# Kernel tuning notes

Measured on AMD Instinct MI355X. Metric: run time of the kernel, lower is better.

Reference implementation:

```python
import jax, jax.numpy as jnp
import numpy as np

M, N, H, K1, K2, C, B = 100000, 14000, 256, 16, 32, 7, 64
EPS = 1e-8


def setup_inputs() -> dict:
    key = jax.random.key(0)
    ks = jax.random.split(key, 8)
    embeds = jax.random.normal(ks[0], (M, H), dtype=jnp.float32)
    idx = jax.random.randint(ks[1], (N,), 0, M, dtype=jnp.int32)
    neighbors = jax.random.randint(ks[2], (N, K1), 0, M, dtype=jnp.int32)
    neighbors_2hop = jax.random.randint(ks[3], (N, K2), 0, M, dtype=jnp.int32)
    labels = (jnp.arange(N, dtype=jnp.int32) % C)  # perfectly balanced, as averageemb requires
    # prompt params (downstreamprompt weights, xavier-uniform [1,H])
    lim = float(np.sqrt(6.0 / (1 + H)))
    w_self = jax.random.uniform(ks[4], (1, H), jnp.float32, -lim, lim)
    w_n = jax.random.uniform(ks[5], (1, H), jnp.float32, -lim, lim)
    w_n2 = jax.random.uniform(ks[6], (1, H), jnp.float32, -lim, lim)
    # metanet (PromptVector): bottleneck adapter H -> B -> H
    k7, k8 = jax.random.split(ks[7])
    W1 = jax.random.normal(k7, (H, B), jnp.float32) * (1.0 / np.sqrt(H))
    b1 = jnp.zeros((B,), jnp.float32)
    W2 = jax.random.normal(k8, (B, H), jnp.float32) * (1.0 / np.sqrt(B))
    b2 = jnp.zeros((H,), jnp.float32)
    return {"embeds": embeds, "w_self": w_self, "w_n": w_n, "w_n2": w_n2,
            "W1": W1, "b1": b1, "W2": W2, "b2": b2,
            "idx": idx, "neighbors": neighbors, "neighbors_2hop": neighbors_2hop,
            "labels": labels}


def _cos(a, b):
    # torch.cosine_similarity with eps=1e-8 (clamped norms)
    num = jnp.sum(a * b, axis=-1)
    na = jnp.maximum(jnp.sqrt(jnp.sum(a * a, axis=-1)), EPS)
    nb = jnp.maximum(jnp.sqrt(jnp.sum(b * b, axis=-1)), EPS)
    return num / (na * nb)


def reference(embeds, w_self, w_n, w_n2, W1, b1, W2, b2,
              idx, neighbors, neighbors_2hop, labels):
    center = embeds[idx]                         # [N,H]
    ce = w_self * center                         # selfprompt: [N,H]
    nb = jnp.nan_to_num(w_n * embeds[neighbors])              # [N,K1,H]
    nb2 = jnp.nan_to_num(w_n2 * embeds[neighbors_2hop])       # [N,K2,H]
    nb_all = jnp.concatenate([nb, nb2], axis=1)  # [N,K1+K2,H]
    sim = _cos(ce[:, None, :], nb_all)           # [N,K]
    w = jax.nn.softmax(sim, axis=-1)
    weighted_neighbors = jnp.einsum('nk,nkh->nh', w, nb_all)
    inputs = weighted_neighbors + ce             # (dropout = identity at eval)
    prompts = jax.nn.elu(inputs @ W1 + b1) @ W2 + b2  # metanet adapter
    rawret = prompts + ce                        # [N,H]
    # averageemb: per-class mean (labels balanced, N/C per class)
    per_class = N // C
    ave = jax.ops.segment_sum(rawret, labels, num_segments=C) / per_class  # [C,H]
    ret = jax.nn.softmax(_cos(rawret[:, None, :], ave[None, :, :]), axis=1)  # [N,C]
    return ret
```

## Files before the change

### kernel.cpp

```cpp
#include <hip/hip_runtime.h>
#include <hip/hip_bf16.h>
#include <math.h>

#define H 256
#define NR 14000
#define MR 100000
#define K1C 16
#define K2C 32
#define KT 48
#define CC 7
#define EPSF 1e-8f
#define GP 448
#define CH2 32

typedef __attribute__((ext_vector_type(8))) unsigned short ushort8_t;

__device__ __forceinline__ float rdlane(float v, int l) {
    return __int_as_float(__builtin_amdgcn_readlane(__float_as_int(v), l));
}

__device__ __forceinline__ float dot4(const float4 a, const float4 b) {
    return a.x * b.x + a.y * b.y + a.z * b.z + a.w * b.w;
}

__device__ __forceinline__ unsigned short f2bf(float x) {
    __hip_bfloat16 h = __float2bfloat16(x);
    return *(unsigned short*)&h;
}

__global__ __launch_bounds__(256) void kE(const float* __restrict__ src,
                                          unsigned short* __restrict__ dst) {
    const size_t base = ((size_t)blockIdx.x * 256 + threadIdx.x) * 8;
    const float4 a = *(const float4*)(src + base);
    const float4 b = *(const float4*)(src + base + 4);
    ushort8_t o;
    o[0] = f2bf(a.x); o[1] = f2bf(a.y); o[2] = f2bf(a.z); o[3] = f2bf(a.w);
    o[4] = f2bf(b.x); o[5] = f2bf(b.y); o[6] = f2bf(b.z); o[7] = f2bf(b.w);
    *(ushort8_t*)(dst + base) = o;
}

__global__ __launch_bounds__(256) void kA3(
    const float* __restrict__ embeds, const unsigned short* __restrict__ ebf,
    const float* __restrict__ w_self, const float* __restrict__ w_n,
    const float* __restrict__ w_n2, const int* __restrict__ idx,
    const int* __restrict__ nbr1, const int* __restrict__ nbr2,
    const float* __restrict__ W1, const float* __restrict__ b1,
    const float* __restrict__ W2, const float* __restrict__ b2,
    float* __restrict__ rawret)
{
    const int tid = threadIdx.x;
    const int wv = tid >> 6, lane = tid & 63;
    const int n = blockIdx.x * 4 + wv;
    const int g = lane >> 4, l = lane & 15;
    const int hb = l * 16;

    float ce[16], wn[16], wn2[16];
    float na2 = 0.f;
    const int cidx = idx[n];
    const float* crow = embeds + (size_t)cidx * H + hb;
#pragma unroll
    for (int j = 0; j < 4; ++j) {
        const float4 wsv  = *(const float4*)(w_self + hb + 4 * j);
        const float4 wnv  = *(const float4*)(w_n    + hb + 4 * j);
        const float4 wn2v = *(const float4*)(w_n2   + hb + 4 * j);
        const float4 cv   = *(const float4*)(crow + 4 * j);
        wn[4*j+0] = wnv.x;  wn[4*j+1] = wnv.y;  wn[4*j+2] = wnv.z;  wn[4*j+3] = wnv.w;
        wn2[4*j+0] = wn2v.x; wn2[4*j+1] = wn2v.y; wn2[4*j+2] = wn2v.z; wn2[4*j+3] = wn2v.w;
        ce[4*j+0] = wsv.x * cv.x; ce[4*j+1] = wsv.y * cv.y;
        ce[4*j+2] = wsv.z * cv.z; ce[4*j+3] = wsv.w * cv.w;
        na2 += ce[4*j+0]*ce[4*j+0] + ce[4*j+1]*ce[4*j+1]
             + ce[4*j+2]*ce[4*j+2] + ce[4*j+3]*ce[4*j+3];
    }
#pragma unroll
    for (int m = 1; m <= 8; m <<= 1) na2 += __shfl_xor(na2, m);
    const float na = fmaxf(sqrtf(na2), EPSF);

    int ridx = 0;
    if (lane < K1C) ridx = nbr1[n * K1C + lane];
    else if (lane < KT) ridx = nbr2[n * K2C + (lane - K1C)];

    float acc[16];
#pragma unroll
    for (int i = 0; i < 16; ++i) acc[i] = 0.f;
    float lsum = 0.f;

#pragma unroll
    for (int kk = 0; kk < 12; ++kk) {
        const int row = __shfl(ridx, kk * 4 + g);
        const unsigned short* rp = ebf + (size_t)row * H + hb;
        const ushort8_t e0 = *(const ushort8_t*)(rp);
        const ushort8_t e1 = *(const ushort8_t*)(rp + 8);
        float nb[16];
#pragma unroll
        for (int i = 0; i < 8; ++i) {
            nb[i]     = __uint_as_float((unsigned)e0[i] << 16);
            nb[8 + i] = __uint_as_float((unsigned)e1[i] << 16);
        }
        float num = 0.f, nn = 0.f;
#pragma unroll
        for (int i = 0; i < 16; ++i) {
            const float w = (kk < 4) ? wn[i] : wn2[i];
            nb[i] *= w;
            num += ce[i] * nb[i];
            nn  += nb[i] * nb[i];
        }
#pragma unroll
        for (int m = 1; m <= 8; m <<= 1) {
            num += __shfl_xor(num, m);
            nn  += __shfl_xor(nn, m);
        }
        const float nbn = fmaxf(sqrtf(nn), EPSF);
        const float e = __expf(num / (nbn * na) - 1.0f);
        lsum += e;
#pragma unroll
        for (int i = 0; i < 16; ++i) acc[i] += e * nb[i];
    }
#pragma unroll
    for (int m = 16; m <= 32; m <<= 1) {
        lsum += __shfl_xor(lsum, m);
#pragma unroll
        for (int i = 0; i < 16; ++i) acc[i] += __shfl_xor(acc[i], m);
    }
    const float rl = 1.0f / lsum;
    float inv[16];
#pragma unroll
    for (int i = 0; i < 16; ++i) inv[i] = acc[i] * rl + ce[i];

    float hid = b1[lane];
    const float* w1p = W1 + lane;
#pragma unroll
    for (int l2 = 0; l2 < 16; ++l2) {
#pragma unroll
        for (int i = 0; i < 16; ++i) {
            const int h = 16 * l2 + i;
            hid = fmaf(rdlane(inv[i], l2), w1p[h * 64], hid);
        }
    }
    hid = hid > 0.f ? hid : (__expf(hid) - 1.0f);

    float p[16];
#pragma unroll
    for (int i = 0; i < 16; ++i) p[i] = 0.f;
    const int gb = lane & 48;
#pragma unroll
    for (int t = 0; t < 16; ++t) {
        const float hv = __shfl(hid, gb + t);
        const float* w2p = W2 + (size_t)(gb + t) * H + hb;
#pragma unroll
        for (int j = 0; j < 4; ++j) {
            const float4 w2v = *(const float4*)(w2p + 4 * j);
            p[4*j+0] = fmaf(hv, w2v.x, p[4*j+0]);
            p[4*j+1] = fmaf(hv, w2v.y, p[4*j+1]);
            p[4*j+2] = fmaf(hv, w2v.z, p[4*j+2]);
            p[4*j+3] = fmaf(hv, w2v.w, p[4*j+3]);
        }
    }
#pragma unroll
    for (int m = 16; m <= 32; m <<= 1) {
#pragma unroll
        for (int i = 0; i < 16; ++i) p[i] += __shfl_xor(p[i], m);
    }

    if (g == 0) {
        float* op = rawret + (size_t)n * H + hb;
#pragma unroll
        for (int j = 0; j < 4; ++j) {
            const float4 b2v = *(const float4*)(b2 + hb + 4 * j);
            float4 ov;
            ov.x = p[4*j+0] + b2v.x + ce[4*j+0];
            ov.y = p[4*j+1] + b2v.y + ce[4*j+1];
            ov.z = p[4*j+2] + b2v.z + ce[4*j+2];
            ov.w = p[4*j+3] + b2v.w + ce[4*j+3];
            *(float4*)(op + 4 * j) = ov;
        }
    }
}

__global__ __launch_bounds__(256) void kC1(
    const float* __restrict__ rawret, const int* __restrict__ labels,
    float* __restrict__ partial)
{
    const int t = threadIdx.x, j = blockIdx.x;
    const int nlo = j * CH2;
    const int nhi = min(nlo + CH2, NR);
    float acc[CC];
#pragma unroll
    for (int c = 0; c < CC; ++c) acc[c] = 0.f;
    for (int n = nlo; n < nhi; n += 4) {
        int lab[4]; float v[4];
#pragma unroll
        for (int u = 0; u < 4; ++u) {
            lab[u] = labels[n + u];
            v[u] = rawret[(size_t)(n + u) * H + t];
        }
#pragma unroll
        for (int u = 0; u < 4; ++u)
#pragma unroll
            for (int c = 0; c < CC; ++c) acc[c] += (lab[u] == c) ? v[u] : 0.f;
    }
#pragma unroll
    for (int c = 0; c < CC; ++c) partial[(size_t)(j * CC + c) * H + t] = acc[c];
}

__global__ __launch_bounds__(256) void kC2(
    const float* __restrict__ partial, float* __restrict__ ave,
    float* __restrict__ anorm)
{
    const int c = blockIdx.x, t = threadIdx.x;
    float s = 0.f;
#pragma unroll 8
    for (int j = 0; j < GP; ++j) s += partial[(size_t)(j * CC + c) * H + t];
    const float a = s * (1.0f / 2000.0f);
    ave[c * H + t] = a;
    __shared__ float red[256];
    red[t] = a * a;
    __syncthreads();
    for (int m = 128; m > 0; m >>= 1) {
        if (t < m) red[t] += red[t + m];
        __syncthreads();
    }
    if (t == 0) anorm[c] = fmaxf(sqrtf(red[0]), EPSF);
}

__global__ __launch_bounds__(256) void kD(
    const float* __restrict__ rawret, const float* __restrict__ ave,
    const float* __restrict__ anorm, float* __restrict__ out)
{
    const int tid = threadIdx.x;
    const int wv = tid >> 6, lane = tid & 63;
    const int n = blockIdx.x * 4 + wv;
    const float4 r4 = *(const float4*)(rawret + (size_t)n * H + 4 * lane);
    float nr2 = dot4(r4, r4);
#pragma unroll
    for (int m = 1; m <= 32; m <<= 1) nr2 += __shfl_xor(nr2, m);
    const float rn = fmaxf(sqrtf(nr2), EPSF);

    float e[CC];
    float s = 0.f;
#pragma unroll
    for (int c = 0; c < CC; ++c) {
        const float4 a4 = *(const float4*)(ave + c * H + 4 * lane);
        float d = dot4(r4, a4);
#pragma unroll
        for (int m = 1; m <= 32; m <<= 1) d += __shfl_xor(d, m);
        const float sim = d / (rn * anorm[c]);
        e[c] = __expf(sim - 1.0f);
        s += e[c];
    }
    const float rs = 1.0f / s;
    if (lane < CC) {
        float v = e[0];
#pragma unroll
        for (int c = 1; c < CC; ++c) v = (lane == c) ? e[c] : v;
        out[(size_t)n * CC + lane] = v * rs;
    }
}

extern "C" void kernel_launch(void* const* d_in, const int* in_sizes, int n_in,
                              void* d_out, int out_size, void* d_ws, size_t ws_size,
                              hipStream_t stream) {
    const float* embeds = (const float*)d_in[0];
    const float* w_self = (const float*)d_in[1];
    const float* w_n    = (const float*)d_in[2];
    const float* w_n2   = (const float*)d_in[3];
    const float* W1     = (const float*)d_in[4];
    const float* b1     = (const float*)d_in[5];
    const float* W2     = (const float*)d_in[6];
    const float* b2     = (const float*)d_in[7];
    const int* idx      = (const int*)d_in[8];
    const int* nbr1     = (const int*)d_in[9];
    const int* nbr2     = (const int*)d_in[10];
    const int* labels   = (const int*)d_in[11];
    float* out = (float*)d_out;

    float* rawret  = (float*)d_ws;
    float* partial = rawret + (size_t)NR * H;
    float* ave     = partial + (size_t)GP * CC * H;
    float* anorm   = ave + (size_t)CC * H;
    unsigned short* ebf = (unsigned short*)(anorm + 8);

    kE<<<(MR * H) / (256 * 8), 256, 0, stream>>>(embeds, ebf);
    kA3<<<NR / 4, 256, 0, stream>>>(embeds, ebf, w_self, w_n, w_n2,
                                    idx, nbr1, nbr2, W1, b1, W2, b2, rawret);
    kC1<<<GP, 256, 0, stream>>>(rawret, labels, partial);
    kC2<<<CC, 256, 0, stream>>>(partial, ave, anorm);
    kD<<<NR / 4, 256, 0, stream>>>(rawret, ave, anorm, out);
}
```

Measured before the change: 358.6 us.

## Split gather and MLP into separate kernels, prefetch neighbor rows, parallelize class reduction

The gather kernel now issues all 12 neighbor-row bf16 loads up front before computing and writes the pre-MLP input and the center embedding to workspace. A new kernel then runs the bottleneck MLP on four rows per wave, so W1/W2 loads are shared across rows. The class-mean reduction uses 56 blocks instead of 7, and the final kernel computes class-mean norms inline instead of reading them from a separate buffer. This adds an extra round trip of two N×H buffers through global memory and raises register pressure from the prefetch buffers.

```diff
diff --git a/kernel.cpp b/kernel.cpp
--- a/kernel.cpp
+++ b/kernel.cpp
@@ -39,14 +39,12 @@
     *(ushort8_t*)(dst + base) = o;
 }
 
-__global__ __launch_bounds__(256) void kA3(
+__global__ __launch_bounds__(256, 2) void kA4(
     const float* __restrict__ embeds, const unsigned short* __restrict__ ebf,
     const float* __restrict__ w_self, const float* __restrict__ w_n,
     const float* __restrict__ w_n2, const int* __restrict__ idx,
     const int* __restrict__ nbr1, const int* __restrict__ nbr2,
-    const float* __restrict__ W1, const float* __restrict__ b1,
-    const float* __restrict__ W2, const float* __restrict__ b2,
-    float* __restrict__ rawret)
+    float* __restrict__ inbuf, float* __restrict__ cebuf)
 {
     const int tid = threadIdx.x;
     const int wv = tid >> 6, lane = tid & 63;
@@ -54,31 +52,49 @@
     const int g = lane >> 4, l = lane & 15;
     const int hb = l * 16;
 
-    float ce[16], wn[16], wn2[16];
-    float na2 = 0.f;
     const int cidx = idx[n];
-    const float* crow = embeds + (size_t)cidx * H + hb;
-#pragma unroll
-    for (int j = 0; j < 4; ++j) {
-        const float4 wsv  = *(const float4*)(w_self + hb + 4 * j);
-        const float4 wnv  = *(const float4*)(w_n    + hb + 4 * j);
-        const float4 wn2v = *(const float4*)(w_n2   + hb + 4 * j);
-        const float4 cv   = *(const float4*)(crow + 4 * j);
-        wn[4*j+0] = wnv.x;  wn[4*j+1] = wnv.y;  wn[4*j+2] = wnv.z;  wn[4*j+3] = wnv.w;
-        wn2[4*j+0] = wn2v.x; wn2[4*j+1] = wn2v.y; wn2[4*j+2] = wn2v.z; wn2[4*j+3] = wn2v.w;
-        ce[4*j+0] = wsv.x * cv.x; ce[4*j+1] = wsv.y * cv.y;
-        ce[4*j+2] = wsv.z * cv.z; ce[4*j+3] = wsv.w * cv.w;
-        na2 += ce[4*j+0]*ce[4*j+0] + ce[4*j+1]*ce[4*j+1]
-             + ce[4*j+2]*ce[4*j+2] + ce[4*j+3]*ce[4*j+3];
-    }
-#pragma unroll
-    for (int m = 1; m <= 8; m <<= 1) na2 += __shfl_xor(na2, m);
-    const float na = fmaxf(sqrtf(na2), EPSF);
-
     int ridx = 0;
     if (lane < K1C) ridx = nbr1[n * K1C + lane];
     else if (lane < KT) ridx = nbr2[n * K2C + (lane - K1C)];
 
+    const float* crow = embeds + (size_t)cidx * H + hb;
+    float4 cv4[4], wsv4[4], wnv4[4], wn2v4[4];
+#pragma unroll
+    for (int j = 0; j < 4; ++j) {
+        cv4[j]   = *(const float4*)(crow + 4 * j);
+        wsv4[j]  = *(const float4*)(w_self + hb + 4 * j);
+        wnv4[j]  = *(const float4*)(w_n    + hb + 4 * j);
+        wn2v4[j] = *(const float4*)(w_n2   + hb + 4 * j);
+    }
+
+    int rows[12];
+#pragma unroll
+    for (int kk = 0; kk < 12; ++kk) rows[kk] = __shfl(ridx, kk * 4 + g);
+    ushort8_t pb[24];
+#pragma unroll
+    for (int kk = 0; kk < 12; ++kk) {
+        const unsigned short* rp = ebf + (size_t)rows[kk] * H + hb;
+        pb[2 * kk]     = *(const ushort8_t*)(rp);
+        pb[2 * kk + 1] = *(const ushort8_t*)(rp + 8);
+    }
+
+    float ce[16], wn[16], wn2[16];
+    float na2 = 0.f;
+#pragma unroll
+    for (int j = 0; j < 4; ++j) {
+        wn[4*j+0] = wnv4[j].x;  wn[4*j+1] = wnv4[j].y;
+        wn[4*j+2] = wnv4[j].z;  wn[4*j+3] = wnv4[j].w;
+        wn2[4*j+0] = wn2v4[j].x; wn2[4*j+1] = wn2v4[j].y;
+        wn2[4*j+2] = wn2v4[j].z; wn2[4*j+3] = wn2v4[j].w;
+        ce[4*j+0] = wsv4[j].x * cv4[j].x; ce[4*j+1] = wsv4[j].y * cv4[j].y;
+        ce[4*j+2] = wsv4[j].z * cv4[j].z; ce[4*j+3] = wsv4[j].w * cv4[j].w;
+        na2 += ce[4*j+0]*ce[4*j+0] + ce[4*j+1]*ce[4*j+1]
+             + ce[4*j+2]*ce[4*j+2] + ce[4*j+3]*ce[4*j+3];
+    }
+#pragma unroll
+    for (int m = 1; m <= 8; m <<= 1) na2 += __shfl_xor(na2, m);
+    const float na = fmaxf(sqrtf(na2), EPSF);
+
     float acc[16];
 #pragma unroll
     for (int i = 0; i < 16; ++i) acc[i] = 0.f;
@@ -86,10 +102,8 @@
 
 #pragma unroll
     for (int kk = 0; kk < 12; ++kk) {
-        const int row = __shfl(ridx, kk * 4 + g);
-        const unsigned short* rp = ebf + (size_t)row * H + hb;
-        const ushort8_t e0 = *(const ushort8_t*)(rp);
-        const ushort8_t e1 = *(const ushort8_t*)(rp + 8);
+        const ushort8_t e0 = pb[2 * kk];
+        const ushort8_t e1 = pb[2 * kk + 1];
         float nb[16];
 #pragma unroll
         for (int i = 0; i < 8; ++i) {
@@ -122,57 +136,65 @@
         for (int i = 0; i < 16; ++i) acc[i] += __shfl_xor(acc[i], m);
     }
     const float rl = 1.0f / lsum;
-    float inv[16];
-#pragma unroll
-    for (int i = 0; i < 16; ++i) inv[i] = acc[i] * rl + ce[i];
-
-    float hid = b1[lane];
-    const float* w1p = W1 + lane;
-#pragma unroll
-    for (int l2 = 0; l2 < 16; ++l2) {
+    if (g == 0) {
+        float* ip = inbuf + (size_t)n * H + hb;
+        float* cp = cebuf + (size_t)n * H + hb;
 #pragma unroll
         for (int i = 0; i < 16; ++i) {
-            const int h = 16 * l2 + i;
-            hid = fmaf(rdlane(inv[i], l2), w1p[h * 64], hid);
-        }
-    }
-    hid = hid > 0.f ? hid : (__expf(hid) - 1.0f);
-
-    float p[16];
-#pragma unroll
-    for (int i = 0; i < 16; ++i) p[i] = 0.f;
-    const int gb = lane & 48;
-#pragma unroll
-    for (int t = 0; t < 16; ++t) {
-        const float hv = __shfl(hid, gb + t);
-        const float* w2p = W2 + (size_t)(gb + t) * H + hb;
-#pragma unroll
-        for (int j = 0; j < 4; ++j) {
-            const float4 w2v = *(const float4*)(w2p + 4 * j);
-            p[4*j+0] = fmaf(hv, w2v.x, p[4*j+0]);
-            p[4*j+1] = fmaf(hv, w2v.y, p[4*j+1]);
-            p[4*j+2] = fmaf(hv, w2v.z, p[4*j+2]);
-            p[4*j+3] = fmaf(hv, w2v.w, p[4*j+3]);
-        }
-    }
-#pragma unroll
-    for (int m = 16; m <= 32; m <<= 1) {
-#pragma unroll
-        for (int i = 0; i < 16; ++i) p[i] += __shfl_xor(p[i], m);
-    }
-
-    if (g == 0) {
-        float* op = rawret + (size_t)n * H + hb;
-#pragma unroll
-        for (int j = 0; j < 4; ++j) {
-            const float4 b2v = *(const float4*)(b2 + hb + 4 * j);
-            float4 ov;
-            ov.x = p[4*j+0] + b2v.x + ce[4*j+0];
-            ov.y = p[4*j+1] + b2v.y + ce[4*j+1];
-            ov.z = p[4*j+2] + b2v.z + ce[4*j+2];
-            ov.w = p[4*j+3] + b2v.w + ce[4*j+3];
-            *(float4*)(op + 4 * j) = ov;
-        }
+            ip[i] = acc[i] * rl + ce[i];
+            cp[i] = ce[i];
+        }
+    }
+}
+
+__global__ __launch_bounds__(256) void kB2(
+    float* __restrict__ io, const float* __restrict__ cebuf,
+    const float* __restrict__ W1, const float* __restrict__ b1,
+    const float* __restrict__ W2, const float* __restrict__ b2)
+{
+    const int tid = threadIdx.x;
+    const int wv = tid >> 6, lane = tid & 63;
+    const int r0 = __builtin_amdgcn_readfirstlane((blockIdx.x * 4 + wv) * 4);
+    const float* inb = io + (size_t)r0 * H;
+
+    float hid[4];
+    const float bb = b1[lane];
+#pragma unroll
+    for (int r = 0; r < 4; ++r) hid[r] = bb;
+
+#pragma unroll 8
+    for (int h = 0; h < 256; ++h) {
+        const float w1v = W1[h * 64 + lane];
+        hid[0] += inb[h]           * w1v;
+        hid[1] += inb[H + h]       * w1v;
+        hid[2] += inb[2 * H + h]   * w1v;
+        hid[3] += inb[3 * H + h]   * w1v;
+    }
+#pragma unroll
+    for (int r = 0; r < 4; ++r)
+        hid[r] = hid[r] > 0.f ? hid[r] : (__expf(hid[r]) - 1.0f);
+
+    float4 p4[4];
+    const float4 b2v = *(const float4*)(b2 + 4 * lane);
+#pragma unroll
+    for (int r = 0; r < 4; ++r) p4[r] = b2v;
+#pragma unroll 4
+    for (int b = 0; b < 64; ++b) {
+        const float4 w2v = *(const float4*)(W2 + b * H + 4 * lane);
+#pragma unroll
+        for (int r = 0; r < 4; ++r) {
+            const float hv = rdlane(hid[r], b);
+            p4[r].x += hv * w2v.x; p4[r].y += hv * w2v.y;
+            p4[r].z += hv * w2v.z; p4[r].w += hv * w2v.w;
+        }
+    }
+#pragma unroll
+    for (int r = 0; r < 4; ++r) {
+        const float4 cev = *(const float4*)(cebuf + (size_t)(r0 + r) * H + 4 * lane);
+        float4 ov;
+        ov.x = p4[r].x + cev.x; ov.y = p4[r].y + cev.y;
+        ov.z = p4[r].z + cev.z; ov.w = p4[r].w + cev.w;
+        *(float4*)(io + (size_t)(r0 + r) * H + 4 * lane) = ov;
     }
 }
 
@@ -203,28 +225,28 @@
 }
 
 __global__ __launch_bounds__(256) void kC2(
-    const float* __restrict__ partial, float* __restrict__ ave,
-    float* __restrict__ anorm)
-{
-    const int c = blockIdx.x, t = threadIdx.x;
-    float s = 0.f;
+    const float* __restrict__ partial, float* __restrict__ ave)
+{
+    const int b = blockIdx.x, c = b >> 3, s = b & 7;
+    const int hloc = threadIdx.x & 31, jg = threadIdx.x >> 5;
+    const int h = 32 * s + hloc;
+    float sum = 0.f;
 #pragma unroll 8
-    for (int j = 0; j < GP; ++j) s += partial[(size_t)(j * CC + c) * H + t];
-    const float a = s * (1.0f / 2000.0f);
-    ave[c * H + t] = a;
+    for (int j = jg; j < GP; j += 8)
+        sum += partial[(size_t)(j * CC + c) * H + h];
     __shared__ float red[256];
-    red[t] = a * a;
+    red[threadIdx.x] = sum;
     __syncthreads();
-    for (int m = 128; m > 0; m >>= 1) {
-        if (t < m) red[t] += red[t + m];
-        __syncthreads();
-    }
-    if (t == 0) anorm[c] = fmaxf(sqrtf(red[0]), EPSF);
-}
-
-__global__ __launch_bounds__(256) void kD(
+    if (jg == 0) {
+#pragma unroll
+        for (int t = 1; t < 8; ++t) sum += red[t * 32 + hloc];
+        ave[c * H + h] = sum * (1.0f / 2000.0f);
+    }
+}
+
+__global__ __launch_bounds__(256) void kD2(
     const float* __restrict__ rawret, const float* __restrict__ ave,
-    const float* __restrict__ anorm, float* __restrict__ out)
+    float* __restrict__ out)
 {
     const int tid = threadIdx.x;
     const int wv = tid >> 6, lane = tid & 63;
@@ -241,9 +263,14 @@
     for (int c = 0; c < CC; ++c) {
         const float4 a4 = *(const float4*)(ave + c * H + 4 * lane);
         float d = dot4(r4, a4);
-#pragma unroll
-        for (int m = 1; m <= 32; m <<= 1) d += __shfl_xor(d, m);
-        const float sim = d / (rn * anorm[c]);
+        float an = dot4(a4, a4);
+#pragma unroll
+        for (int m = 1; m <= 32; m <<= 1) {
+            d  += __shfl_xor(d, m);
+            an += __shfl_xor(an, m);
+        }
+        const float anorm = fmaxf(sqrtf(an), EPSF);
+        const float sim = d / (rn * anorm);
         e[c] = __expf(sim - 1.0f);
         s += e[c];
     }
@@ -274,15 +301,16 @@
     float* out = (float*)d_out;
 
     float* rawret  = (float*)d_ws;
-    float* partial = rawret + (size_t)NR * H;
+    float* cebuf   = rawret + (size_t)NR * H;
+    float* partial = cebuf + (size_t)NR * H;
     float* ave     = partial + (size_t)GP * CC * H;
-    float* anorm   = ave + (size_t)CC * H;
-    unsigned short* ebf = (unsigned short*)(anorm + 8);
+    unsigned short* ebf = (unsigned short*)(ave + CC * H + 8);
 
     kE<<<(MR * H) / (256 * 8), 256, 0, stream>>>(embeds, ebf);
-    kA3<<<NR / 4, 256, 0, stream>>>(embeds, ebf, w_self, w_n, w_n2,
-                                    idx, nbr1, nbr2, W1, b1, W2, b2, rawret);
+    kA4<<<NR / 4, 256, 0, stream>>>(embeds, ebf, w_self, w_n, w_n2,
+                                    idx, nbr1, nbr2, rawret, cebuf);
+    kB2<<<NR / 16, 256, 0, stream>>>(rawret, cebuf, W1, b1, W2, b2);
     kC1<<<GP, 256, 0, stream>>>(rawret, labels, partial);
-    kC2<<<CC, 256, 0, stream>>>(partial, ave, anorm);
-    kD<<<NR / 4, 256, 0, stream>>>(rawret, ave, anorm, out);
-}
+    kC2<<<56, 256, 0, stream>>>(partial, ave);
+    kD2<<<NR / 4, 256, 0, stream>>>(rawret, ave, out);
+}
```

After: 308.7 us. -13.9%, faster.
